# Kernel optimization log

Hardware: AMD Instinct MI355X
Metric: run time of the kernel (lower is better)

## Reference

```python
import jax, jax.numpy as jnp
import numpy as np

# dims: B=batch, CIN/COUT=channels, T=timesteps, K=kernel length (= T+1, since
# max_timesteps=2048 is even and CKConv bumps it to odd), DK=SIREN hidden width
B, CIN, COUT, T, DK = 32, 32, 32, 2048, 32
K = T + 1


def setup_inputs() -> dict:
    key = jax.random.key(0)
    ks = jax.random.split(key, 9)
    u = lambda k, shape, lim: jax.random.uniform(k, shape, minval=-lim, maxval=lim)
    # SIREN layer 1 (Conv1d 1->DK, k=1): first layer init uniform(-1, 1)
    w1 = u(ks[0], (DK, 1), 1.0)
    b1 = u(ks[1], (DK,), 1.0)          # torch bias init: U(-1/sqrt(fan_in)), fan_in=1
    # SIREN layer 2 (DK->DK): uniform(-sqrt(6/DK)/omega0, +), omega0=1
    siren_val = float(np.sqrt(6.0 / DK))
    w2 = u(ks[2], (DK, DK), siren_val)
    b2 = u(ks[3], (DK,), float(1.0 / np.sqrt(DK)))
    # output layer (DK -> CIN*COUT)
    w3 = u(ks[4], (CIN * COUT, DK), siren_val)
    b3 = u(ks[5], (CIN * COUT,), float(1.0 / np.sqrt(DK)))
    omega1 = jnp.asarray(1.0, jnp.float32)
    omega2 = jnp.asarray(1.0, jnp.float32)
    bias = jax.random.normal(ks[6], (COUT,), jnp.float32)   # CKConv output bias
    x = jax.random.normal(ks[7], (B, CIN, T), jnp.float32)
    rel_pos = jnp.linspace(-1.0, 1.0, K, dtype=jnp.float32)  # buffer _rel_positions
    return dict(x=x, rel_pos=rel_pos, w1=w1, b1=b1, omega1=omega1,
                w2=w2, b2=b2, omega2=omega2, w3=w3, b3=b3, bias=bias)


def reference(x, rel_pos, w1, b1, omega1, w2, b2, omega2, w3, b3, bias):
    # --- SIREN kernel network: 1x1 convs over the K positions == matmuls ---
    pos = rel_pos[None, :]                                   # (1, K)
    h = jnp.sin(omega1 * (w1 @ pos + b1[:, None]))           # (DK, K)
    h = jnp.sin(omega2 * (w2 @ h + b2[:, None]))             # (DK, K)
    kern = (w3 @ h + b3[:, None]).reshape(COUT, CIN, K)      # (COUT, CIN, K)
    # --- causal conv: left-pad by K-1 zeros, then valid cross-correlation ---
    out = jax.lax.conv_general_dilated(
        x, kern, window_strides=(1,), padding=[(K - 1, 0)],
        dimension_numbers=("NCH", "OIH", "NCH"))             # (B, COUT, T)
    return out + bias[None, :, None]
```

## Files before the change

### kernel.cpp

```cpp
#include <hip/hip_runtime.h>
#include <hip/hip_bf16.h>
#include <stdint.h>

typedef short bf16x8 __attribute__((ext_vector_type(8)));
typedef float f32x16 __attribute__((ext_vector_type(16)));
typedef uint32_t u32x2 __attribute__((ext_vector_type(2), aligned(4)));

#define T 2048
#define KLEN 2049
#define DK 32
#define NCO 32
#define NCI 32
#define NB 32

#define GR 2216
#define SREF 2055
#define WT_CH 257
#define WT_ELEMS (NCI*WT_CH*NCO*8)
#define XR_ELEMS (NB*NCI*GR)

#define WT_OFF 0
#define XR_OFF (WT_ELEMS*2)
#define XRS_OFF (XR_OFF + XR_ELEMS*2)

#define CIB 528
#define GPC 1056
#define GPCP 1088
#define CPYB 17472
#define BUFB (2*CPYB)
#define LDS_TOT (2*BUFB)

#define GENX_BLOCKS ((NB*NCI*GR)/256)

__global__ __launch_bounds__(256) void gen(
    const float* __restrict__ rel_pos,
    const float* __restrict__ w1, const float* __restrict__ b1, const float* __restrict__ om1,
    const float* __restrict__ w2, const float* __restrict__ b2, const float* __restrict__ om2,
    const float* __restrict__ w3, const float* __restrict__ b3,
    const float* __restrict__ x,
    uint16_t* __restrict__ Wt, uint16_t* __restrict__ xr, uint16_t* __restrict__ xrs)
{
    __shared__ float h1s[8][32];
    __shared__ float h2s[8][32];
    int t = threadIdx.x;
    if (blockIdx.x < WT_CH) {
        int dchunk = blockIdx.x;
        int dd = t >> 5, i = t & 31;
        int d = (dchunk << 3) + dd;
        float pos = (d < KLEN) ? rel_pos[2048 - d] : 0.f;
        h1s[dd][i] = sinf(om1[0] * (w1[i] * pos + b1[i]));
        __syncthreads();
        {
            float a = b2[i];
            #pragma unroll
            for (int j = 0; j < 32; ++j) a += w2[i*32 + j] * h1s[dd][j];
            h2s[dd][i] = sinf(om2[0] * a);
        }
        __syncthreads();
        for (int r = 0; r < 4; ++r) {
            int tt = t + (r << 8);
            int ci = tt >> 5, co = tt & 31;
            int coci = (co << 5) + ci;
            float w3r[32];
            #pragma unroll
            for (int j = 0; j < 8; ++j)
                *(float4*)&w3r[j*4] = *(const float4*)&w3[coci*32 + j*4];
            float bb = b3[coci];
            union { uint16_t u[8]; uint4 qv; } pack;
            #pragma unroll
            for (int ddd = 0; ddd < 8; ++ddd) {
                float a = bb;
                #pragma unroll
                for (int j = 0; j < 32; ++j) a += w3r[j] * h2s[ddd][j];
                if (((dchunk << 3) + ddd) >= KLEN) a = 0.f;
                __hip_bfloat16 hv = __float2bfloat16(a);
                pack.u[ddd] = *(uint16_t*)&hv;
            }
            *(uint4*)&Wt[((ci*WT_CH + dchunk)*NCO + co) << 3] = pack.qv;
        }
    } else {
        int idx = (blockIdx.x - WT_CH)*256 + t;
        if (idx >= NB*NCI*GR) return;
        int row = idx / GR;
        int g = idx - row*GR;
        int s = SREF - g;
        float v  = (s  >= 0 && s  < T) ? x[row*T + s]  : 0.f;
        int s2 = s - 1;
        float v2 = (s2 >= 0 && s2 < T) ? x[row*T + s2] : 0.f;
        __hip_bfloat16 hv = __float2bfloat16(v);
        __hip_bfloat16 hv2 = __float2bfloat16(v2);
        xr[idx]  = *(uint16_t*)&hv;
        xrs[idx] = *(uint16_t*)&hv2;
    }
}

__device__ __forceinline__ void gld16(const uint16_t* g, char* l)
{
    typedef const __attribute__((address_space(1))) uint32_t GU;
    typedef __attribute__((address_space(3))) uint32_t LU;
    __builtin_amdgcn_global_load_lds((GU*)g, (LU*)l, 16, 0, 0);
}

__global__ __launch_bounds__(512, 4) void conv(
    const uint16_t* __restrict__ Wt, const uint16_t* __restrict__ xr,
    const float* __restrict__ bias, float* __restrict__ out)
{
    __shared__ uint4 lds4[LDS_TOT/16];
    char* ldsb = (char*)lds4;
    float* red = (float*)lds4;
    int tid = threadIdx.x;
    int b = blockIdx.x & 31;
    int q = blockIdx.x >> 5;
    int p = q & 7;
    int th = (q < 8) ? (63 - (p << 2)) : ((p << 2) + 3);
    int nw = (th + 1) >> 2;
    int g0base = 2016 - (th << 5);
    int w = tid >> 6, lane = tid & 63, n = lane & 31, hi = lane >> 5;
    int cig = w;

    int srcE[5], dstC[5];
    #pragma unroll
    for (int k = 0; k < 5; ++k) {
        int gi = tid + (k << 9);
        if (gi < 2176) {
            int cpy = gi >= GPCP;
            int j = gi - cpy*GPCP;
            dstC[k] = cpy*CPYB + (j << 4);
            if (j < GPC) {
                int ci = (j*1986) >> 16;
                int qq = j - ci*33;
                srcE[k] = (cpy ? XR_ELEMS : 0) + (b*NCI + ci)*GR + (qq << 3);
            } else srcE[k] = 0;
        } else { srcE[k] = 0; dstC[k] = -1; }
    }

    int obase = 39 - n + (hi << 3);
    int par = obase & 1;
    int bbb = cig*CIB + par*CPYB + ((obase - par) << 1);

    f32x16 acc0, acc1, acc2, acc3;
    #pragma unroll
    for (int r = 0; r < 16; ++r) { acc0[r]=0.f; acc1[r]=0.f; acc2[r]=0.f; acc3[r]=0.f; }

    #define STAGE(BUF, GOFF) { \
        _Pragma("unroll") \
        for (int k = 0; k < 5; ++k) \
            if (dstC[k] >= 0) gld16(xr + srcE[k] + (GOFF), (BUF) + dstC[k]); }

    STAGE(ldsb, g0base)
    __syncthreads();

    for (int wi = 0; wi < nw; ++wi) {
        int cur = wi & 1;
        if (wi + 1 < nw) {
            char* bufn = ldsb + (cur ^ 1)*BUFB;
            int g0n = g0base + ((wi + 1) << 7);
            STAGE(bufn, g0n)
        }
        int dcw = wi << 4;
        const char* rbase = ldsb + cur*BUFB + bbb;

        __builtin_amdgcn_s_setprio(1);
        #pragma unroll
        for (int cii = 0; cii < 4; ++cii) {
            int ci = (cii << 3) + cig;
            const uint16_t* aB = Wt + (((ci*WT_CH + dcw + hi)*NCO + n) << 3);
            bf16x8 av0 = *(const bf16x8*)(aB);
            bf16x8 av1 = *(const bf16x8*)(aB + 512);
            bf16x8 av2 = *(const bf16x8*)(aB + 1024);
            bf16x8 av3 = *(const bf16x8*)(aB + 1536);
            bf16x8 av4 = *(const bf16x8*)(aB + 2048);
            bf16x8 av5 = *(const bf16x8*)(aB + 2560);
            bf16x8 av6 = *(const bf16x8*)(aB + 3072);
            bf16x8 av7 = *(const bf16x8*)(aB + 3584);
            const char* pbase = rbase + cii*(8*CIB);

            #define LOADF(DST, MM) { \
                const char* pp = pbase + ((MM) << 5); \
                (DST).d[0] = *(const u32x2*)(pp); \
                (DST).d[1] = *(const u32x2*)(pp + 8); }
            #define MF(AC, AV, BV) AC = __builtin_amdgcn_mfma_f32_32x32x16_bf16(AV, BV, AC, 0,0,0);

            union FB { u32x2 d[2]; bf16x8 v; } f0, f1;
            LOADF(f0, 0)
            LOADF(f1, 1)
            MF(acc0, av0, f0.v)                                          LOADF(f0, 2)
            MF(acc0, av1, f1.v)                                          LOADF(f1, 3)
            MF(acc0, av2, f0.v) MF(acc1, av0, f0.v)                      LOADF(f0, 4)
            MF(acc0, av3, f1.v) MF(acc1, av1, f1.v)                      LOADF(f1, 5)
            MF(acc0, av4, f0.v) MF(acc1, av2, f0.v) MF(acc2, av0, f0.v)  LOADF(f0, 6)
            MF(acc0, av5, f1.v) MF(acc1, av3, f1.v) MF(acc2, av1, f1.v)  LOADF(f1, 7)
            MF(acc0, av6, f0.v) MF(acc1, av4, f0.v) MF(acc2, av2, f0.v) MF(acc3, av0, f0.v) LOADF(f0, 8)
            MF(acc0, av7, f1.v) MF(acc1, av5, f1.v) MF(acc2, av3, f1.v) MF(acc3, av1, f1.v) LOADF(f1, 9)
            MF(acc1, av6, f0.v) MF(acc2, av4, f0.v) MF(acc3, av2, f0.v)  LOADF(f0, 10)
            MF(acc1, av7, f1.v) MF(acc2, av5, f1.v) MF(acc3, av3, f1.v)  LOADF(f1, 11)
            MF(acc2, av6, f0.v) MF(acc3, av4, f0.v)                      LOADF(f0, 12)
            MF(acc2, av7, f1.v) MF(acc3, av5, f1.v)                      LOADF(f1, 13)
            MF(acc3, av6, f0.v)
            MF(acc3, av7, f1.v)
            #undef MF
            #undef LOADF
        }
        __builtin_amdgcn_s_setprio(0);
        __syncthreads();
    }
    #undef STAGE

    #pragma unroll
    for (int dlt = 0; dlt < 4; ++dlt) {
        f32x16 a = (dlt == 0) ? acc0 : (dlt == 1) ? acc1 : (dlt == 2) ? acc2 : acc3;
        __syncthreads();
        if (w < 4) {
            #pragma unroll
            for (int r = 0; r < 16; ++r)
                red[(w*16 + r)*64 + lane] = a[r];
        }
        __syncthreads();
        if (w >= 4) {
            #pragma unroll
            for (int r = 0; r < 16; ++r)
                red[((w-4)*16 + r)*64 + lane] += a[r];
        }
        __syncthreads();
        int t0 = (th - dlt) << 5;
        #pragma unroll
        for (int h = 0; h < 2; ++h) {
            int e = tid + (h << 9);
            int lane_e = e & 63;
            int reg = e >> 6;
            float s = 0.f;
            #pragma unroll
            for (int ww = 0; ww < 4; ++ww) s += red[(ww*16 + reg)*64 + lane_e];
            int co = (reg & 3) + ((reg >> 2) << 3) + ((lane_e >> 5) << 2);
            int t = t0 + (lane_e & 31);
            out[(b*NCO + co)*T + t] = s + bias[co];
        }
    }
}

extern "C" void kernel_launch(void* const* d_in, const int* in_sizes, int n_in,
                              void* d_out, int out_size, void* d_ws, size_t ws_size,
                              hipStream_t stream)
{
    const float* x       = (const float*)d_in[0];
    const float* rel_pos = (const float*)d_in[1];
    const float* w1  = (const float*)d_in[2];
    const float* b1  = (const float*)d_in[3];
    const float* om1 = (const float*)d_in[4];
    const float* w2  = (const float*)d_in[5];
    const float* b2  = (const float*)d_in[6];
    const float* om2 = (const float*)d_in[7];
    const float* w3  = (const float*)d_in[8];
    const float* b3  = (const float*)d_in[9];
    const float* bias = (const float*)d_in[10];
    float* out = (float*)d_out;
    char* ws = (char*)d_ws;
    uint16_t* Wt  = (uint16_t*)(ws + WT_OFF);
    uint16_t* xrp = (uint16_t*)(ws + XR_OFF);
    uint16_t* xrs = (uint16_t*)(ws + XRS_OFF);

    hipLaunchKernelGGL(gen, dim3(WT_CH + GENX_BLOCKS), dim3(256), 0, stream,
                       rel_pos, w1, b1, om1, w2, b2, om2, w3, b3, x, Wt, xrp, xrs);
    hipLaunchKernelGGL(conv, dim3(NB*16), dim3(512), 0, stream, Wt, xrp, bias, out);
}
```

Measured before the change: 161.4 us.

## Give each wave private LDS staging and replace block barriers with vmcnt waits

The conv kernel's LDS staging is reorganized so each wave loads only the input rows for its own channel group into a private double buffer. Block-wide __syncthreads in the main loop are replaced with per-wave s_waitcnt vmcnt, and the s_setprio calls are removed. The aim is to let waves run independently instead of stalling on barriers. The gen kernel is also split into separate weight and input preparation launches, which adds one kernel launch. The correctness of the new buffer offsets and wait counts is not obvious: the fifth gld16 writes at offset 3200 and overlaps the fourth chunk's range. The per-wave waitcnt also relies on the global_load_lds completion semantics, since other waves no longer sync before reading.

Result: faster. 154.4 us (-4.3%).

```diff
diff --git a/kernel.cpp b/kernel.cpp
--- a/kernel.cpp
+++ b/kernel.cpp
@@ -23,75 +23,72 @@
 #define XR_OFF (WT_ELEMS*2)
 #define XRS_OFF (XR_OFF + XR_ELEMS*2)
 
-#define CIB 528
-#define GPC 1056
-#define GPCP 1088
-#define CPYB 17472
-#define BUFB (2*CPYB)
-#define LDS_TOT (2*BUFB)
-
-#define GENX_BLOCKS ((NB*NCI*GR)/256)
-
-__global__ __launch_bounds__(256) void gen(
+#define WBUF 4352
+#define WREG (2*WBUF)
+#define LDS_TOT (8*WREG)
+
+__global__ __launch_bounds__(256) void gen_w(
     const float* __restrict__ rel_pos,
     const float* __restrict__ w1, const float* __restrict__ b1, const float* __restrict__ om1,
     const float* __restrict__ w2, const float* __restrict__ b2, const float* __restrict__ om2,
     const float* __restrict__ w3, const float* __restrict__ b3,
-    const float* __restrict__ x,
-    uint16_t* __restrict__ Wt, uint16_t* __restrict__ xr, uint16_t* __restrict__ xrs)
+    uint16_t* __restrict__ Wt)
 {
     __shared__ float h1s[8][32];
     __shared__ float h2s[8][32];
     int t = threadIdx.x;
-    if (blockIdx.x < WT_CH) {
-        int dchunk = blockIdx.x;
-        int dd = t >> 5, i = t & 31;
-        int d = (dchunk << 3) + dd;
-        float pos = (d < KLEN) ? rel_pos[2048 - d] : 0.f;
-        h1s[dd][i] = sinf(om1[0] * (w1[i] * pos + b1[i]));
-        __syncthreads();
-        {
-            float a = b2[i];
-            #pragma unroll
-            for (int j = 0; j < 32; ++j) a += w2[i*32 + j] * h1s[dd][j];
-            h2s[dd][i] = sinf(om2[0] * a);
-        }
-        __syncthreads();
-        for (int r = 0; r < 4; ++r) {
-            int tt = t + (r << 8);
-            int ci = tt >> 5, co = tt & 31;
-            int coci = (co << 5) + ci;
-            float w3r[32];
-            #pragma unroll
-            for (int j = 0; j < 8; ++j)
-                *(float4*)&w3r[j*4] = *(const float4*)&w3[coci*32 + j*4];
-            float bb = b3[coci];
-            union { uint16_t u[8]; uint4 qv; } pack;
-            #pragma unroll
-            for (int ddd = 0; ddd < 8; ++ddd) {
-                float a = bb;
-                #pragma unroll
-                for (int j = 0; j < 32; ++j) a += w3r[j] * h2s[ddd][j];
-                if (((dchunk << 3) + ddd) >= KLEN) a = 0.f;
-                __hip_bfloat16 hv = __float2bfloat16(a);
-                pack.u[ddd] = *(uint16_t*)&hv;
-            }
-            *(uint4*)&Wt[((ci*WT_CH + dchunk)*NCO + co) << 3] = pack.qv;
-        }
-    } else {
-        int idx = (blockIdx.x - WT_CH)*256 + t;
-        if (idx >= NB*NCI*GR) return;
-        int row = idx / GR;
-        int g = idx - row*GR;
-        int s = SREF - g;
-        float v  = (s  >= 0 && s  < T) ? x[row*T + s]  : 0.f;
-        int s2 = s - 1;
-        float v2 = (s2 >= 0 && s2 < T) ? x[row*T + s2] : 0.f;
-        __hip_bfloat16 hv = __float2bfloat16(v);
-        __hip_bfloat16 hv2 = __float2bfloat16(v2);
-        xr[idx]  = *(uint16_t*)&hv;
-        xrs[idx] = *(uint16_t*)&hv2;
-    }
+    int dchunk = blockIdx.x;
+    int dd = t >> 5, i = t & 31;
+    int d = (dchunk << 3) + dd;
+    float pos = (d < KLEN) ? rel_pos[2048 - d] : 0.f;
+    h1s[dd][i] = sinf(om1[0] * (w1[i] * pos + b1[i]));
+    __syncthreads();
+    {
+        float a = b2[i];
+        #pragma unroll
+        for (int j = 0; j < 32; ++j) a += w2[i*32 + j] * h1s[dd][j];
+        h2s[dd][i] = sinf(om2[0] * a);
+    }
+    __syncthreads();
+    for (int r = 0; r < 4; ++r) {
+        int tt = t + (r << 8);
+        int ci = tt >> 5, co = tt & 31;
+        int coci = (co << 5) + ci;
+        float w3r[32];
+        #pragma unroll
+        for (int j = 0; j < 8; ++j)
+            *(float4*)&w3r[j*4] = *(const float4*)&w3[coci*32 + j*4];
+        float bb = b3[coci];
+        union { uint16_t u[8]; uint4 qv; } pack;
+        #pragma unroll
+        for (int ddd = 0; ddd < 8; ++ddd) {
+            float a = bb;
+            #pragma unroll
+            for (int j = 0; j < 32; ++j) a += w3r[j] * h2s[ddd][j];
+            if (((dchunk << 3) + ddd) >= KLEN) a = 0.f;
+            __hip_bfloat16 hv = __float2bfloat16(a);
+            pack.u[ddd] = *(uint16_t*)&hv;
+        }
+        *(uint4*)&Wt[((ci*WT_CH + dchunk)*NCO + co) << 3] = pack.qv;
+    }
+}
+
+__global__ __launch_bounds__(256) void gen_x(const float* __restrict__ x,
+                                             uint16_t* __restrict__ xr,
+                                             uint16_t* __restrict__ xrs)
+{
+    int idx = blockIdx.x*256 + threadIdx.x;
+    if (idx >= NB*NCI*GR) return;
+    int row = idx / GR;
+    int g = idx - row*GR;
+    int s = SREF - g;
+    float v  = (s  >= 0 && s  < T) ? x[row*T + s]  : 0.f;
+    int s2 = s - 1;
+    float v2 = (s2 >= 0 && s2 < T) ? x[row*T + s2] : 0.f;
+    __hip_bfloat16 hv = __float2bfloat16(v);
+    __hip_bfloat16 hv2 = __float2bfloat16(v2);
+    xr[idx]  = *(uint16_t*)&hv;
+    xrs[idx] = *(uint16_t*)&hv2;
 }
 
 __device__ __forceinline__ void gld16(const uint16_t* g, char* l)
@@ -117,50 +114,49 @@
     int g0base = 2016 - (th << 5);
     int w = tid >> 6, lane = tid & 63, n = lane & 31, hi = lane >> 5;
     int cig = w;
-
-    int srcE[5], dstC[5];
+    char* wbase = ldsb + w*WREG;
+
+    int srcE[5];
     #pragma unroll
     for (int k = 0; k < 5; ++k) {
-        int gi = tid + (k << 9);
-        if (gi < 2176) {
-            int cpy = gi >= GPCP;
-            int j = gi - cpy*GPCP;
-            dstC[k] = cpy*CPYB + (j << 4);
-            if (j < GPC) {
-                int ci = (j*1986) >> 16;
-                int qq = j - ci*33;
-                srcE[k] = (cpy ? XR_ELEMS : 0) + (b*NCI + ci)*GR + (qq << 3);
-            } else srcE[k] = 0;
-        } else { srcE[k] = 0; dstC[k] = -1; }
+        int g = (k < 4) ? (k*64 + lane) : (200 + lane);
+        int cpy = g >= 132;
+        int r = g - 132*cpy;
+        int cl = (r*1986) >> 16;
+        int qq = r - cl*33;
+        srcE[k] = cpy*XR_ELEMS + (b*NCI + (cl << 3) + cig)*GR + (qq << 3);
     }
 
     int obase = 39 - n + (hi << 3);
     int par = obase & 1;
-    int bbb = cig*CIB + par*CPYB + ((obase - par) << 1);
+    int bbb = par*2112 + ((obase - par) << 1);
 
     f32x16 acc0, acc1, acc2, acc3;
     #pragma unroll
     for (int r = 0; r < 16; ++r) { acc0[r]=0.f; acc1[r]=0.f; acc2[r]=0.f; acc3[r]=0.f; }
 
-    #define STAGE(BUF, GOFF) { \
-        _Pragma("unroll") \
-        for (int k = 0; k < 5; ++k) \
-            if (dstC[k] >= 0) gld16(xr + srcE[k] + (GOFF), (BUF) + dstC[k]); }
-
-    STAGE(ldsb, g0base)
-    __syncthreads();
+    #define STAGEW(BUF, GOFF) { \
+        gld16(xr + srcE[0] + (GOFF), (BUF));          \
+        gld16(xr + srcE[1] + (GOFF), (BUF) + 1024);   \
+        gld16(xr + srcE[2] + (GOFF), (BUF) + 2048);   \
+        gld16(xr + srcE[3] + (GOFF), (BUF) + 3072);   \
+        gld16(xr + srcE[4] + (GOFF), (BUF) + 3200); }
+
+    STAGEW(wbase, g0base)
 
     for (int wi = 0; wi < nw; ++wi) {
         int cur = wi & 1;
         if (wi + 1 < nw) {
-            char* bufn = ldsb + (cur ^ 1)*BUFB;
+            char* bufn = wbase + (cur ^ 1)*WBUF;
             int g0n = g0base + ((wi + 1) << 7);
-            STAGE(bufn, g0n)
+            STAGEW(bufn, g0n)
+            asm volatile("s_waitcnt vmcnt(5)" ::: "memory");
+        } else {
+            asm volatile("s_waitcnt vmcnt(0)" ::: "memory");
         }
         int dcw = wi << 4;
-        const char* rbase = ldsb + cur*BUFB + bbb;
-
-        __builtin_amdgcn_s_setprio(1);
+        const char* rbase = wbase + cur*WBUF + bbb;
+
         #pragma unroll
         for (int cii = 0; cii < 4; ++cii) {
             int ci = (cii << 3) + cig;
@@ -173,7 +169,7 @@
             bf16x8 av5 = *(const bf16x8*)(aB + 2560);
             bf16x8 av6 = *(const bf16x8*)(aB + 3072);
             bf16x8 av7 = *(const bf16x8*)(aB + 3584);
-            const char* pbase = rbase + cii*(8*CIB);
+            const char* pbase = rbase + cii*528;
 
             #define LOADF(DST, MM) { \
                 const char* pp = pbase + ((MM) << 5); \
@@ -201,10 +197,8 @@
             #undef MF
             #undef LOADF
         }
-        __builtin_amdgcn_s_setprio(0);
-        __syncthreads();
-    }
-    #undef STAGE
+    }
+    #undef STAGEW
 
     #pragma unroll
     for (int dlt = 0; dlt < 4; ++dlt) {
@@ -259,7 +253,9 @@
     uint16_t* xrp = (uint16_t*)(ws + XR_OFF);
     uint16_t* xrs = (uint16_t*)(ws + XRS_OFF);
 
-    hipLaunchKernelGGL(gen, dim3(WT_CH + GENX_BLOCKS), dim3(256), 0, stream,
-                       rel_pos, w1, b1, om1, w2, b2, om2, w3, b3, x, Wt, xrp, xrs);
+    hipLaunchKernelGGL(gen_w, dim3(WT_CH), dim3(256), 0, stream,
+                       rel_pos, w1, b1, om1, w2, b2, om2, w3, b3, Wt);
+    int n2 = NB*NCI*GR;
+    hipLaunchKernelGGL(gen_x, dim3((n2+255)/256), dim3(256), 0, stream, x, xrp, xrs);
     hipLaunchKernelGGL(conv, dim3(NB*16), dim3(512), 0, stream, Wt, xrp, bias, out);
 }
```
